# Kernel tuning notes

Measured on AMD Instinct MI355X. Metric: run time of the kernel, lower is better.

Reference implementation:

```python
import jax, jax.numpy as jnp
import numpy as np

B, N, C = 8, 4096, 768
H = 12
D = C // H  # 64


def setup_inputs() -> dict:
    key = jax.random.key(0)
    k1, k2, k3 = jax.random.split(key, 3)
    x = jax.random.normal(k1, (B, N, C), dtype=jnp.float32)
    Wqkv = jax.random.normal(k2, (C, 3 * C), dtype=jnp.float32) * (C ** -0.5)
    Wproj = jax.random.normal(k3, (C, C), dtype=jnp.float32) * (C ** -0.5)
    bproj = jnp.zeros((C,), dtype=jnp.float32)
    return {"x": x, "Wqkv": Wqkv, "Wproj": Wproj, "bproj": bproj}


def reference(x, Wqkv, Wproj, bproj):
    b, n, c = x.shape
    qkv = x @ Wqkv  # [B,N,3C]
    qkv = qkv.reshape(b, n, 3, H, D).transpose(2, 0, 3, 1, 4)  # [3,B,H,N,D]
    q, k, v = qkv[0], qkv[1], qkv[2]
    # softmax over the sequence axis (dim=-2 in torch => N)
    k = jax.nn.softmax(k, axis=-2)
    # context: [B,H,D,D] -- small d x d intermediate
    context = jnp.einsum('bhnd,bhne->bhde', k, v)
    out = jnp.einsum('bhnd,bhde->bhne', q, context)  # [B,H,N,D]
    out = out.transpose(0, 2, 1, 3).reshape(b, n, c)  # b h n d -> b n (h d)
    return out @ Wproj + bproj
```

## Files before the change

kernel.cpp:

```cpp
#include <hip/hip_runtime.h>
#include <cstdint>
#include <cstddef>


typedef __bf16 bf8_t __attribute__((ext_vector_type(8)));
typedef float f4_t __attribute__((ext_vector_type(4)));

#define DEV_INLINE __device__ __forceinline__

DEV_INLINE void gload16(const void* g, void* l) {
  __builtin_amdgcn_global_load_lds(
      (const __attribute__((address_space(1))) void*)g,
      (__attribute__((address_space(3))) void*)l, 16, 0, 0);
}

__global__ __launch_bounds__(256) void cast_f32_bf16(const float* __restrict__ in,
                                                     __bf16* __restrict__ out, int n4) {
  int i = blockIdx.x * 256 + threadIdx.x;
  if (i >= n4) return;
  float4 f = ((const float4*)in)[i];
  union { __bf16 h[4]; uint2 u; } o;
  o.h[0] = (__bf16)f.x; o.h[1] = (__bf16)f.y; o.h[2] = (__bf16)f.z; o.h[3] = (__bf16)f.w;
  ((uint2*)out)[i] = o.u;
}

__global__ __launch_bounds__(256) void transpose_cast(const float* __restrict__ in,
                                                      __bf16* __restrict__ out, int R, int C) {
  int o = blockIdx.x * 256 + threadIdx.x;
  if (o >= R * C) return;
  int c = o / R, r = o - c * R;
  out[o] = (__bf16)in[r * C + c];
}

__global__ __launch_bounds__(256) void gemm1_qkv(const __bf16* __restrict__ A,
                                                 const __bf16* __restrict__ B,
                                                 __bf16* __restrict__ Qo,
                                                 __bf16* __restrict__ KTo,
                                                 __bf16* __restrict__ VTo) {
  constexpr int LDA = 768, LDB = 768, BK = 32, KTOT = 768, NT = 18;
  __shared__ __bf16 sA[128 * 32];
  __shared__ __bf16 sB[128 * 32];
  const int tid = threadIdx.x;
  const int mt = blockIdx.x / NT, nt = blockIdx.x % NT;
  const int lane = tid & 63, wv = tid >> 6;
  const int wr = (wv >> 1) * 64, wc = (wv & 1) * 64;
  const int lr = lane & 15, quad = lane >> 4;

  const int e0 = tid * 8;
  const int srow = e0 >> 5, skk = e0 & 31;
  const __bf16* gA = A + (size_t)(mt * 128 + srow) * LDA + skk;
  const __bf16* gB = B + (size_t)(nt * 128 + srow) * LDB + skk;

  const f4_t fz = {0.f, 0.f, 0.f, 0.f};
  f4_t acc[4][4];
#pragma unroll
  for (int i = 0; i < 4; i++)
#pragma unroll
    for (int j = 0; j < 4; j++) acc[i][j] = fz;

  for (int k0 = 0; k0 < KTOT; k0 += BK) {
    gload16(gA, &sA[e0]);
    gload16(gA + 64 * LDA, &sA[e0 + 2048]);
    gload16(gB, &sB[e0]);
    gload16(gB + 64 * LDB, &sB[e0 + 2048]);
    gA += BK; gB += BK;
    __syncthreads();
    bf8_t af[4], bfm[4];
#pragma unroll
    for (int i = 0; i < 4; i++)
      af[i] = *(const bf8_t*)&sA[(wr + i * 16 + lr) * 32 + quad * 8];
#pragma unroll
    for (int j = 0; j < 4; j++)
      bfm[j] = *(const bf8_t*)&sB[(wc + j * 16 + lr) * 32 + quad * 8];
#pragma unroll
    for (int i = 0; i < 4; i++)
#pragma unroll
      for (int j = 0; j < 4; j++)
        acc[i][j] = __builtin_amdgcn_mfma_f32_16x16x32_bf16(af[i], bfm[j], acc[i][j], 0, 0, 0);
    __syncthreads();
  }

  const int s = nt / 6;
  const int colw0 = (nt % 6) * 128 + wc;
  const int row0 = mt * 128 + wr;
  if (s == 0) {
#pragma unroll
    for (int i = 0; i < 4; i++)
#pragma unroll
      for (int j = 0; j < 4; j++) {
        int col = colw0 + j * 16 + lr;
#pragma unroll
        for (int r = 0; r < 4; r++)
          Qo[(size_t)(row0 + i * 16 + quad * 4 + r) * 768 + col] = (__bf16)acc[i][j][r];
      }
  } else {
    __bf16* T = (s == 1) ? KTo : VTo;
    const int b = row0 >> 12;
    const int n0 = (row0 & 4095) + quad * 4;
#pragma unroll
    for (int i = 0; i < 4; i++) {
      int n = n0 + i * 16;
#pragma unroll
      for (int j = 0; j < 4; j++) {
        int cw = colw0 + j * 16 + lr;
        int h = cw >> 6, d = cw & 63;
        union { __bf16 h4[4]; uint2 u; } pk;
#pragma unroll
        for (int r = 0; r < 4; r++) pk.h4[r] = (__bf16)acc[i][j][r];
        *(uint2*)&T[((size_t)(b * 12 + h) * 64 + d) * 4096 + n] = pk.u;
      }
    }
  }
}

__global__ __launch_bounds__(256) void softmax_rows(__bf16* __restrict__ KT) {
  __shared__ float red[8];
  __bf16* p = KT + (size_t)blockIdx.x * 4096;
  const int tid = threadIdx.x, lane = tid & 63, wv = tid >> 6;
  bf8_t x0 = *(const bf8_t*)&p[tid * 16];
  bf8_t x1 = *(const bf8_t*)&p[tid * 16 + 8];
  float v[16];
#pragma unroll
  for (int k = 0; k < 8; k++) { v[k] = (float)x0[k]; v[8 + k] = (float)x1[k]; }
  float m = v[0];
#pragma unroll
  for (int k = 1; k < 16; k++) m = fmaxf(m, v[k]);
  for (int o = 32; o; o >>= 1) m = fmaxf(m, __shfl_xor(m, o, 64));
  if (lane == 0) red[wv] = m;
  __syncthreads();
  m = fmaxf(fmaxf(red[0], red[1]), fmaxf(red[2], red[3]));
  float s = 0.f;
#pragma unroll
  for (int k = 0; k < 16; k++) { v[k] = __expf(v[k] - m); s += v[k]; }
  for (int o = 32; o; o >>= 1) s += __shfl_xor(s, o, 64);
  if (lane == 0) red[4 + wv] = s;
  __syncthreads();
  s = red[4] + red[5] + red[6] + red[7];
  float inv = 1.0f / s;
  bf8_t o0, o1;
#pragma unroll
  for (int k = 0; k < 8; k++) { o0[k] = (__bf16)(v[k] * inv); o1[k] = (__bf16)(v[8 + k] * inv); }
  *(bf8_t*)&p[tid * 16] = o0;
  *(bf8_t*)&p[tid * 16 + 8] = o1;
}

__global__ __launch_bounds__(256) void ctx_kernel(const __bf16* __restrict__ KT,
                                                  const __bf16* __restrict__ VT,
                                                  float* __restrict__ part) {
  const int bh = blockIdx.x >> 3, kc = blockIdx.x & 7;
  const int tid = threadIdx.x, lane = tid & 63, wv = tid >> 6;
  const int wr = (wv >> 1) * 32, wc = (wv & 1) * 32;
  const int lr = lane & 15, quad = lane >> 4;
  const __bf16* Ab = KT + (size_t)bh * 64 * 4096;
  const __bf16* Bb = VT + (size_t)bh * 64 * 4096;
  const f4_t fz = {0.f, 0.f, 0.f, 0.f};
  f4_t acc[2][2] = {{fz, fz}, {fz, fz}};
  const int kbeg = kc * 512;
  for (int k0 = kbeg; k0 < kbeg + 512; k0 += 32) {
    bf8_t a[2], b[2];
#pragma unroll
    for (int i = 0; i < 2; i++)
      a[i] = *(const bf8_t*)&Ab[(size_t)(wr + i * 16 + lr) * 4096 + k0 + quad * 8];
#pragma unroll
    for (int j = 0; j < 2; j++)
      b[j] = *(const bf8_t*)&Bb[(size_t)(wc + j * 16 + lr) * 4096 + k0 + quad * 8];
#pragma unroll
    for (int i = 0; i < 2; i++)
#pragma unroll
      for (int j = 0; j < 2; j++)
        acc[i][j] = __builtin_amdgcn_mfma_f32_16x16x32_bf16(a[i], b[j], acc[i][j], 0, 0, 0);
  }
  float* po = part + (size_t)blockIdx.x * 4096;
#pragma unroll
  for (int i = 0; i < 2; i++)
#pragma unroll
    for (int j = 0; j < 2; j++)
#pragma unroll
      for (int r = 0; r < 4; r++)
        po[(wr + i * 16 + quad * 4 + r) * 64 + wc + j * 16 + lr] = acc[i][j][r];
}

__global__ __launch_bounds__(256) void wfused_kernel(const float* __restrict__ part,
                                                     const __bf16* __restrict__ WpT,
                                                     __bf16* __restrict__ B2T) {
  __shared__ __bf16 sctx[64 * 64];
  const int bh = blockIdx.x, cblk = blockIdx.y;
  const int b = bh / 12, h = bh % 12;
  const int tid = threadIdx.x;
  for (int i = tid; i < 4096; i += 256) {
    float s = 0.f;
#pragma unroll
    for (int kc = 0; kc < 8; kc++) s += part[(size_t)(bh * 8 + kc) * 4096 + i];
    sctx[i] = (__bf16)s;
  }
  __syncthreads();
  const int lane = tid & 63, wv = tid >> 6, lr = lane & 15, quad = lane >> 4;
  const int c0 = cblk * 192 + wv * 48;
  const f4_t fz = {0.f, 0.f, 0.f, 0.f};
  f4_t acc[3][4];
#pragma unroll
  for (int i = 0; i < 3; i++)
#pragma unroll
    for (int j = 0; j < 4; j++) acc[i][j] = fz;
#pragma unroll
  for (int k0 = 0; k0 < 64; k0 += 32) {
    bf8_t a[3], bq[4];
#pragma unroll
    for (int i = 0; i < 3; i++)
      a[i] = *(const bf8_t*)&WpT[(size_t)(c0 + i * 16 + lr) * 768 + h * 64 + k0 + quad * 8];
#pragma unroll
    for (int j = 0; j < 4; j++)
      bq[j] = *(const bf8_t*)&sctx[(j * 16 + lr) * 64 + k0 + quad * 8];
#pragma unroll
    for (int i = 0; i < 3; i++)
#pragma unroll
      for (int j = 0; j < 4; j++)
        acc[i][j] = __builtin_amdgcn_mfma_f32_16x16x32_bf16(a[i], bq[j], acc[i][j], 0, 0, 0);
  }
#pragma unroll
  for (int i = 0; i < 3; i++)
#pragma unroll
    for (int j = 0; j < 4; j++)
#pragma unroll
      for (int r = 0; r < 4; r++) {
        int c = c0 + i * 16 + quad * 4 + r;
        int d = j * 16 + lr;
        B2T[((size_t)b * 768 + c) * 768 + h * 64 + d] = (__bf16)acc[i][j][r];
      }
}

__global__ __launch_bounds__(256) void gemm2_out(const __bf16* __restrict__ A,
                                                 const __bf16* __restrict__ Ball,
                                                 float* __restrict__ C,
                                                 const float* __restrict__ bias) {
  constexpr int LDA = 768, LDB = 768, BK = 32, KTOT = 768, NT = 6;
  __shared__ __bf16 sA[128 * 32];
  __shared__ __bf16 sB[128 * 32];
  const int tid = threadIdx.x;
  const int mt = blockIdx.x / NT, nt = blockIdx.x % NT;
  const __bf16* B = Ball + (size_t)(mt >> 5) * 768 * 768;
  const int lane = tid & 63, wv = tid >> 6;
  const int wr = (wv >> 1) * 64, wc = (wv & 1) * 64;
  const int lr = lane & 15, quad = lane >> 4;

  const int e0 = tid * 8;
  const int srow = e0 >> 5, skk = e0 & 31;
  const __bf16* gA = A + (size_t)(mt * 128 + srow) * LDA + skk;
  const __bf16* gB = B + (size_t)(nt * 128 + srow) * LDB + skk;

  const f4_t fz = {0.f, 0.f, 0.f, 0.f};
  f4_t acc[4][4];
#pragma unroll
  for (int i = 0; i < 4; i++)
#pragma unroll
    for (int j = 0; j < 4; j++) acc[i][j] = fz;

  for (int k0 = 0; k0 < KTOT; k0 += BK) {
    gload16(gA, &sA[e0]);
    gload16(gA + 64 * LDA, &sA[e0 + 2048]);
    gload16(gB, &sB[e0]);
    gload16(gB + 64 * LDB, &sB[e0 + 2048]);
    gA += BK; gB += BK;
    __syncthreads();
    bf8_t af[4], bfm[4];
#pragma unroll
    for (int i = 0; i < 4; i++)
      af[i] = *(const bf8_t*)&sA[(wr + i * 16 + lr) * 32 + quad * 8];
#pragma unroll
    for (int j = 0; j < 4; j++)
      bfm[j] = *(const bf8_t*)&sB[(wc + j * 16 + lr) * 32 + quad * 8];
#pragma unroll
    for (int i = 0; i < 4; i++)
#pragma unroll
      for (int j = 0; j < 4; j++)
        acc[i][j] = __builtin_amdgcn_mfma_f32_16x16x32_bf16(af[i], bfm[j], acc[i][j], 0, 0, 0);
    __syncthreads();
  }

  const int row0 = mt * 128 + wr;
  const int col0 = nt * 128 + wc;
#pragma unroll
  for (int j = 0; j < 4; j++) {
    int col = col0 + j * 16 + lr;
    float bv = bias[col];
#pragma unroll
    for (int i = 0; i < 4; i++)
#pragma unroll
      for (int r = 0; r < 4; r++)
        C[(size_t)(row0 + i * 16 + quad * 4 + r) * 768 + col] = acc[i][j][r] + bv;
  }
}

extern "C" void kernel_launch(void* const* d_in, const int* in_sizes, int n_in,
                              void* d_out, int out_size, void* d_ws, size_t ws_size,
                              hipStream_t stream) {
  const float* x = (const float*)d_in[0];
  const float* Wqkv = (const float*)d_in[1];
  const float* Wproj = (const float*)d_in[2];
  const float* bproj = (const float*)d_in[3];
  float* out = (float*)d_out;

  char* ws = (char*)d_ws;
  __bf16* Xb   = (__bf16*)(ws + 0);
  float*  part = (float*)(ws + 0);
  __bf16* B2T  = (__bf16*)(ws + 12582912);
  __bf16* WqkvT = (__bf16*)(ws + 50331648);
  __bf16* WpT   = (__bf16*)(ws + 53870592);
  __bf16* Q     = (__bf16*)(ws + 55050240);
  __bf16* KT    = (__bf16*)(ws + 105381888);
  __bf16* VT    = (__bf16*)(ws + 155713536);

  cast_f32_bf16<<<24576, 256, 0, stream>>>(x, Xb, 25165824 / 4);
  transpose_cast<<<(768 * 2304) / 256, 256, 0, stream>>>(Wqkv, WqkvT, 768, 2304);
  transpose_cast<<<(768 * 768) / 256, 256, 0, stream>>>(Wproj, WpT, 768, 768);
  gemm1_qkv<<<256 * 18, 256, 0, stream>>>(Xb, WqkvT, Q, KT, VT);
  softmax_rows<<<6144, 256, 0, stream>>>(KT);
  ctx_kernel<<<96 * 8, 256, 0, stream>>>(KT, VT, part);
  wfused_kernel<<<dim3(96, 4), 256, 0, stream>>>(part, WpT, B2T);
  gemm2_out<<<256 * 6, 256, 0, stream>>>(Q, B2T, out, bproj);
}
```

Before: 469.9 us.

## Fold Q projection into per-batch combined output weight to skip Q GEMM

Stops computing Q explicitly. The per-batch matrix (context·Wproj) is pre-multiplied by Wq in a new small combine kernel, and the final GEMM reads X directly. This removes one third of the large QKV GEMM and the Q write and read through HBM. In exchange it adds a per-batch 768x768x768 GEMM and an extra bf16 rounding of the combined weight, which may shift numerical accuracy.

```diff
diff --git a/kernel.cpp b/kernel.cpp
--- a/kernel.cpp
+++ b/kernel.cpp
@@ -32,12 +32,18 @@
   out[o] = (__bf16)in[r * C + c];
 }
 
-__global__ __launch_bounds__(256) void gemm1_qkv(const __bf16* __restrict__ A,
-                                                 const __bf16* __restrict__ B,
-                                                 __bf16* __restrict__ Qo,
-                                                 __bf16* __restrict__ KTo,
-                                                 __bf16* __restrict__ VTo) {
-  constexpr int LDA = 768, LDB = 768, BK = 32, KTOT = 768, NT = 18;
+__global__ __launch_bounds__(256) void wq_cast(const float* __restrict__ in,
+                                               __bf16* __restrict__ out) {
+  int o = blockIdx.x * 256 + threadIdx.x;
+  int r = o / 768, c = o - r * 768;
+  out[o] = (__bf16)in[r * 2304 + c];
+}
+
+__global__ __launch_bounds__(256) void gemm1_kv(const __bf16* __restrict__ A,
+                                                const __bf16* __restrict__ B,
+                                                __bf16* __restrict__ KTo,
+                                                __bf16* __restrict__ VTo) {
+  constexpr int LDA = 768, LDB = 768, BK = 32, KTOT = 768, NT = 12;
   __shared__ __bf16 sA[128 * 32];
   __shared__ __bf16 sB[128 * 32];
   const int tid = threadIdx.x;
@@ -83,32 +89,20 @@
   const int s = nt / 6;
   const int colw0 = (nt % 6) * 128 + wc;
   const int row0 = mt * 128 + wr;
-  if (s == 0) {
-#pragma unroll
-    for (int i = 0; i < 4; i++)
-#pragma unroll
-      for (int j = 0; j < 4; j++) {
-        int col = colw0 + j * 16 + lr;
-#pragma unroll
-        for (int r = 0; r < 4; r++)
-          Qo[(size_t)(row0 + i * 16 + quad * 4 + r) * 768 + col] = (__bf16)acc[i][j][r];
-      }
-  } else {
-    __bf16* T = (s == 1) ? KTo : VTo;
-    const int b = row0 >> 12;
-    const int n0 = (row0 & 4095) + quad * 4;
-#pragma unroll
-    for (int i = 0; i < 4; i++) {
-      int n = n0 + i * 16;
-#pragma unroll
-      for (int j = 0; j < 4; j++) {
-        int cw = colw0 + j * 16 + lr;
-        int h = cw >> 6, d = cw & 63;
-        union { __bf16 h4[4]; uint2 u; } pk;
-#pragma unroll
-        for (int r = 0; r < 4; r++) pk.h4[r] = (__bf16)acc[i][j][r];
-        *(uint2*)&T[((size_t)(b * 12 + h) * 64 + d) * 4096 + n] = pk.u;
-      }
+  __bf16* T = (s == 0) ? KTo : VTo;
+  const int b = row0 >> 12;
+  const int n0 = (row0 & 4095) + quad * 4;
+#pragma unroll
+  for (int i = 0; i < 4; i++) {
+    int n = n0 + i * 16;
+#pragma unroll
+    for (int j = 0; j < 4; j++) {
+      int cw = colw0 + j * 16 + lr;
+      int h = cw >> 6, d = cw & 63;
+      union { __bf16 h4[4]; uint2 u; } pk;
+#pragma unroll
+      for (int r = 0; r < 4; r++) pk.h4[r] = (__bf16)acc[i][j][r];
+      *(uint2*)&T[((size_t)(b * 12 + h) * 64 + d) * 4096 + n] = pk.u;
     }
   }
 }
@@ -227,6 +221,58 @@
         int d = j * 16 + lr;
         B2T[((size_t)b * 768 + c) * 768 + h * 64 + d] = (__bf16)acc[i][j][r];
       }
+}
+
+__global__ __launch_bounds__(256) void combine_kernel(const __bf16* __restrict__ B2Tall,
+                                                      const __bf16* __restrict__ Wq,
+                                                      __bf16* __restrict__ Wcomb) {
+  constexpr int LD = 768, BK = 32, KTOT = 768;
+  __shared__ __bf16 sA[64 * 32];
+  __shared__ __bf16 sB[64 * 32];
+  const int b = blockIdx.x / 144, rem = blockIdx.x % 144;
+  const int mt = rem / 12, nt = rem % 12;
+  const __bf16* A = B2Tall + (size_t)b * 768 * 768;
+  const int tid = threadIdx.x, lane = tid & 63, wv = tid >> 6;
+  const int wr = (wv >> 1) * 32, wc = (wv & 1) * 32;
+  const int lr = lane & 15, quad = lane >> 4;
+
+  const int e0 = tid * 8;
+  const int srow = e0 >> 5, skk = e0 & 31;
+  const __bf16* gA = A + (size_t)(mt * 64 + srow) * LD + skk;
+  const __bf16* gB = Wq + (size_t)(nt * 64 + srow) * LD + skk;
+
+  const f4_t fz = {0.f, 0.f, 0.f, 0.f};
+  f4_t acc[2][2] = {{fz, fz}, {fz, fz}};
+
+  for (int k0 = 0; k0 < KTOT; k0 += BK) {
+    gload16(gA, &sA[e0]);
+    gload16(gB, &sB[e0]);
+    gA += BK; gB += BK;
+    __syncthreads();
+    bf8_t a[2], bq[2];
+#pragma unroll
+    for (int i = 0; i < 2; i++)
+      a[i] = *(const bf8_t*)&sA[(wr + i * 16 + lr) * 32 + quad * 8];
+#pragma unroll
+    for (int j = 0; j < 2; j++)
+      bq[j] = *(const bf8_t*)&sB[(wc + j * 16 + lr) * 32 + quad * 8];
+#pragma unroll
+    for (int i = 0; i < 2; i++)
+#pragma unroll
+      for (int j = 0; j < 2; j++)
+        acc[i][j] = __builtin_amdgcn_mfma_f32_16x16x32_bf16(a[i], bq[j], acc[i][j], 0, 0, 0);
+    __syncthreads();
+  }
+  __bf16* C = Wcomb + (size_t)b * 768 * 768;
+  const int row0 = mt * 64 + wr, col0 = nt * 64 + wc;
+#pragma unroll
+  for (int i = 0; i < 2; i++)
+#pragma unroll
+    for (int j = 0; j < 2; j++)
+#pragma unroll
+      for (int r = 0; r < 4; r++)
+        C[(size_t)(row0 + i * 16 + quad * 4 + r) * 768 + col0 + j * 16 + lr] =
+            (__bf16)acc[i][j][r];
 }
 
 __global__ __launch_bounds__(256) void gemm2_out(const __bf16* __restrict__ A,
@@ -301,21 +347,24 @@
   float* out = (float*)d_out;
 
   char* ws = (char*)d_ws;
-  __bf16* Xb   = (__bf16*)(ws + 0);
-  float*  part = (float*)(ws + 0);
-  __bf16* B2T  = (__bf16*)(ws + 12582912);
-  __bf16* WqkvT = (__bf16*)(ws + 50331648);
-  __bf16* WpT   = (__bf16*)(ws + 53870592);
-  __bf16* Q     = (__bf16*)(ws + 55050240);
-  __bf16* KT    = (__bf16*)(ws + 105381888);
-  __bf16* VT    = (__bf16*)(ws + 155713536);
+  __bf16* Xb    = (__bf16*)(ws + 0);
+  __bf16* KT    = (__bf16*)(ws + 50331648);
+  __bf16* VT    = (__bf16*)(ws + 100663296);
+  __bf16* WqkvT = (__bf16*)(ws + 150994944);
+  __bf16* Wqc   = (__bf16*)(ws + 154533888);
+  __bf16* WpT   = (__bf16*)(ws + 155713536);
+  float*  part  = (float*)(ws + 156893184);
+  __bf16* B2T   = (__bf16*)(ws + 169476096);
+  __bf16* Wcomb = (__bf16*)(ws + 178913280);
 
   cast_f32_bf16<<<24576, 256, 0, stream>>>(x, Xb, 25165824 / 4);
   transpose_cast<<<(768 * 2304) / 256, 256, 0, stream>>>(Wqkv, WqkvT, 768, 2304);
+  wq_cast<<<(768 * 768) / 256, 256, 0, stream>>>(Wqkv, Wqc);
   transpose_cast<<<(768 * 768) / 256, 256, 0, stream>>>(Wproj, WpT, 768, 768);
-  gemm1_qkv<<<256 * 18, 256, 0, stream>>>(Xb, WqkvT, Q, KT, VT);
+  gemm1_kv<<<256 * 12, 256, 0, stream>>>(Xb, WqkvT + 768 * 768, KT, VT);
   softmax_rows<<<6144, 256, 0, stream>>>(KT);
   ctx_kernel<<<96 * 8, 256, 0, stream>>>(KT, VT, part);
   wfused_kernel<<<dim3(96, 4), 256, 0, stream>>>(part, WpT, B2T);
-  gemm2_out<<<256 * 6, 256, 0, stream>>>(Q, B2T, out, bproj);
-}
+  combine_kernel<<<1152, 256, 0, stream>>>(B2T, Wqc, Wcomb);
+  gemm2_out<<<256 * 6, 256, 0, stream>>>(Xb, Wcomb, out, bproj);
+}
```

New measurement: 450.6 us. 1.04x faster.
